# Performance work log

Measured on AMD Instinct MI355X. Metric: run time of the kernel, lower is better.

The kernel has to match this reference:

```python
import jax, jax.numpy as jnp
import numpy as np

NEG_SLOPE = 0.2
EPS = 1e-16  # PyG softmax denominator epsilon


def _gatv2_layer(x, src, dst, n_nodes, W_l, W_r, att, bias):
    """Single-head GATv2Conv (PyG defaults, self loops already in src/dst).
    x: [N, F_in]; src/dst: [E]; W_l/W_r: [F_in, F_out]; att: [F_out]; bias: [F_out].
    """
    x_l = x @ W_l                       # source transform [N, F_out]
    x_r = x @ W_r                       # target transform [N, F_out]
    # per-edge attention logit: a^T LeakyReLU(x_l[j] + x_r[i])
    e = jax.nn.leaky_relu(x_l[src] + x_r[dst], NEG_SLOPE) @ att  # [E]
    # softmax over incoming edges of each destination node
    e_max = jax.ops.segment_max(e, dst, num_segments=n_nodes)    # [N]
    ex = jnp.exp(e - e_max[dst])                                  # [E]
    denom = jax.ops.segment_sum(ex, dst, num_segments=n_nodes)   # [N]
    alpha = ex / (denom[dst] + EPS)                               # [E]
    out = jax.ops.segment_sum(alpha[:, None] * x_l[src], dst, num_segments=n_nodes)
    return out + bias


def setup_inputs() -> dict:
    key = jax.random.key(0)
    N, E = 50000, 800000
    IN, HID, OUT = 128, 64, 64
    ks = jax.random.split(key, 12)
    x = jax.random.normal(ks[0], (N, IN), dtype=jnp.float32)
    edge_index = jax.random.randint(ks[1], (2, E), 0, N, dtype=jnp.int64)
    s1 = float(1.0 / np.sqrt(IN))
    s2 = float(1.0 / np.sqrt(HID))
    return {
        "x": x,
        "edge_index": edge_index,
        "W1_l": jax.random.uniform(ks[2], (IN, HID), jnp.float32, -s1, s1),
        "W1_r": jax.random.uniform(ks[3], (IN, HID), jnp.float32, -s1, s1),
        "att1": jax.random.uniform(ks[4], (HID,), jnp.float32, -s2, s2),
        "b1": jnp.zeros((HID,), jnp.float32),
        "W2_l": jax.random.uniform(ks[5], (HID, OUT), jnp.float32, -s2, s2),
        "W2_r": jax.random.uniform(ks[6], (HID, OUT), jnp.float32, -s2, s2),
        "att2": jax.random.uniform(ks[7], (OUT,), jnp.float32, -s2, s2),
        "b2": jnp.zeros((OUT,), jnp.float32),
    }


def reference(x, edge_index, W1_l, W1_r, att1, b1, W2_l, W2_r, att2, b2):
    n = x.shape[0]
    loop = jnp.arange(n, dtype=edge_index.dtype)
    src = jnp.concatenate([edge_index[0], loop])  # add self loops (PyG default)
    dst = jnp.concatenate([edge_index[1], loop])
    h = _gatv2_layer(x, src, dst, n, W1_l, W1_r, att1, b1)
    h = jax.nn.relu(h)
    out = _gatv2_layer(h, src, dst, n, W2_l, W2_r, att2, b2)
    return out
```

## Files before the change

kernel.cpp:

```cpp
#include <hip/hip_runtime.h>
#include <math.h>

#define NEG_SLOPE 0.2f
#define EPSV 1e-16f
#define NEG_HUGE -1e30f
#define CAP 64
#define GH 1024

typedef short short8 __attribute__((ext_vector_type(8)));
typedef float f32x4 __attribute__((ext_vector_type(4)));
typedef unsigned short u16;


__global__ __launch_bounds__(256) void k_wpack(
        const float* __restrict__ W1l, const float* __restrict__ W1r,
        const float* __restrict__ W2l, const float* __restrict__ W2r,
        u16* __restrict__ w1hi, u16* __restrict__ w1lo,
        u16* __restrict__ w2hi, u16* __restrict__ w2lo,
        int* __restrict__ cnt, u16* __restrict__ csrc, int N, int NP) {
    const int idx = blockIdx.x * 256 + threadIdx.x;
    const int G = gridDim.x * 256;
    const int CN = 8 * NP;
    for (int i = idx; i < CN; i += G) {
        const int cls = i / NP;
        const int r = i - cls * NP;
        const int d = r * 8 + cls;
        cnt[i] = (d < N) ? 1 : 0;
    }
    for (int d = idx; d < N; d += G) csrc[(size_t)d * CAP] = (u16)d;
    const int T1 = 128 * 128, T2 = 64 * 128;
    if (idx >= T1 + T2) return;
    u16 *dhi, *dlo; const float *Wl, *Wr; int li;
    if (idx < T1) { dhi = w1hi; dlo = w1lo; Wl = W1l; Wr = W1r; li = idx; }
    else          { dhi = w2hi; dlo = w2lo; Wl = W2l; Wr = W2r; li = idx - T1; }
    const int j = li & 7, l = (li >> 3) & 63, t = (li >> 9) & 7, c = li >> 12;
    const int k = c * 32 + (l >> 4) * 8 + j;
    const int n = t * 16 + (l & 15);
    const float v = (n < 64) ? Wl[k * 64 + n] : Wr[k * 64 + (n - 64)];
    const unsigned u = __float_as_uint(v);
    dhi[li] = (u16)(u >> 16);
    const float hif = __uint_as_float(u & 0xffff0000u);
    dlo[li] = (u16)(__float_as_uint(v - hif) >> 16);
}

__device__ __forceinline__ void split8(const float* fs, short8& ahi, short8& alo) {
#pragma unroll
    for (int j = 0; j < 8; ++j) {
        const unsigned u = __float_as_uint(fs[j]);
        ahi[j] = (short)(u >> 16);
        const float hif = __uint_as_float(u & 0xffff0000u);
        alo[j] = (short)(__float_as_uint(fs[j] - hif) >> 16);
    }
}

template <int K>
__device__ __forceinline__ void gemm_mfma_tile(const float* __restrict__ X,
                                               const u16* __restrict__ whi,
                                               const u16* __restrict__ wlo,
                                               float* __restrict__ xl,
                                               float* __restrict__ xr,
                                               int N, int tile) {
    const int lane = threadIdx.x & 63;
    const int w = threadIdx.x >> 6;
    const int rowbase = tile * 64 + w * 16;
    const int m = lane & 15, q = lane >> 4;
    int ar = rowbase + m; if (ar > N - 1) ar = N - 1;
    const float* arow = X + (size_t)ar * K + q * 8;
    f32x4 acc[8];
#pragma unroll
    for (int t = 0; t < 8; ++t) acc[t] = (f32x4){0.f, 0.f, 0.f, 0.f};
#pragma unroll
    for (int c = 0; c < K / 32; ++c) {
        const f32x4 f0 = __builtin_nontemporal_load((const f32x4*)(arow + c * 32));
        const f32x4 f1 = __builtin_nontemporal_load((const f32x4*)(arow + c * 32 + 4));
        const float fs[8] = {f0[0], f0[1], f0[2], f0[3], f1[0], f1[1], f1[2], f1[3]};
        short8 ahi, alo;
        split8(fs, ahi, alo);
        const u16* bp = whi + ((size_t)(c * 8) * 64 + lane) * 8;
        const u16* bq = wlo + ((size_t)(c * 8) * 64 + lane) * 8;
#pragma unroll
        for (int t = 0; t < 8; ++t) {
            const short8 bhi = *(const short8*)(bp + t * 64 * 8);
            const short8 blo = *(const short8*)(bq + t * 64 * 8);
            acc[t] = __builtin_amdgcn_mfma_f32_16x16x32_bf16(bhi, ahi, acc[t], 0, 0, 0);
            acc[t] = __builtin_amdgcn_mfma_f32_16x16x32_bf16(blo, ahi, acc[t], 0, 0, 0);
            acc[t] = __builtin_amdgcn_mfma_f32_16x16x32_bf16(bhi, alo, acc[t], 0, 0, 0);
        }
    }
    const int row = rowbase + m;
    if (row < N) {
#pragma unroll
        for (int t = 0; t < 8; ++t) {
            const int colb = t * 16 + q * 4;
            float* dstp = (t < 4) ? (xl + (size_t)row * 64 + colb)
                                  : (xr + (size_t)row * 64 + (colb - 64));
            __builtin_nontemporal_store(acc[t], (f32x4*)dstp);
        }
    }
}

template <int K>
__global__ __launch_bounds__(256) void k_hist_gemm(const int* __restrict__ ei, int E,
                                                   int* __restrict__ cnt,
                                                   u16* __restrict__ csrc,
                                                   const float* __restrict__ X,
                                                   const u16* __restrict__ whi,
                                                   const u16* __restrict__ wlo,
                                                   float* __restrict__ xl,
                                                   float* __restrict__ xr,
                                                   int N, int NP) {
    if ((int)blockIdx.x < GH) {
        const int cls = blockIdx.x & 7;
        const int stripe = blockIdx.x >> 3;
        const int NS = GH >> 3;
        const int tid = threadIdx.x;
        const int* srcp = ei;
        const int* dstp = ei + E;
        int* cntc = cnt + cls * NP;
        if ((E & 7) == 0) {
            for (int base = stripe * 2048; base < E; base += NS * 2048) {
                const int e8 = base + tid * 8;
                if (e8 < E) {
                    const int4 da = *(const int4*)(dstp + e8);
                    const int4 db = *(const int4*)(dstp + e8 + 4);
                    const int4 sa = *(const int4*)(srcp + e8);
                    const int4 sb = *(const int4*)(srcp + e8 + 4);
                    const int d[8] = {da.x, da.y, da.z, da.w, db.x, db.y, db.z, db.w};
                    const int s[8] = {sa.x, sa.y, sa.z, sa.w, sb.x, sb.y, sb.z, sb.w};
                    bool m[8]; int sl[8];
#pragma unroll
                    for (int j = 0; j < 8; ++j) {
                        m[j] = (d[j] & 7) == cls;
                        if (m[j]) sl[j] = atomicAdd(&cntc[d[j] >> 3], 1);
                    }
#pragma unroll
                    for (int j = 0; j < 8; ++j) {
                        if (m[j]) csrc[(size_t)d[j] * CAP + sl[j]] = (u16)s[j];
                    }
                }
            }
        } else {
            for (int base = stripe * 256; base < E; base += NS * 256) {
                const int e = base + tid;
                if (e < E) {
                    const int dd = dstp[e];
                    if ((dd & 7) == cls) {
                        const int ss = srcp[e];
                        const int slot = atomicAdd(&cntc[dd >> 3], 1);
                        csrc[(size_t)dd * CAP + slot] = (u16)ss;
                    }
                }
            }
        }
    } else {
        gemm_mfma_tile<K>(X, whi, wlo, xl, xr, N, blockIdx.x - GH);
    }
}

template <int K>
__global__ __launch_bounds__(256) void k_gemm(const float* __restrict__ X,
                                              const u16* __restrict__ whi,
                                              const u16* __restrict__ wlo,
                                              float* __restrict__ xl,
                                              float* __restrict__ xr, int N) {
    gemm_mfma_tile<K>(X, whi, wlo, xl, xr, N, blockIdx.x);
}

__global__ __launch_bounds__(256) void k_attn(const float* __restrict__ xl,
                                              const float* xr,
                                              const float* __restrict__ att,
                                              const int* __restrict__ cnt,
                                              const u16* __restrict__ csrc,
                                              const float* __restrict__ bias,
                                              float* out, int N, int NP, int relu) {
    const int lane = threadIdx.x & 63;
    const int g = lane >> 4;
    const int i = lane & 15;
    const int dst = blockIdx.x * 4 + (threadIdx.x >> 6);
    if (dst >= N) return;
    const float4 xrv = *(const float4*)(xr + (size_t)dst * 64 + i * 4);
    const float4 aw  = *(const float4*)(att + i * 4);
    const int deg = cnt[(dst & 7) * NP + (dst >> 3)];
    const int sidx = (int)csrc[(size_t)dst * CAP + ((lane < deg) ? lane : 0)];
    float l = 0.0f;
    float4 acc = {0.0f, 0.0f, 0.0f, 0.0f};
    for (int t = 0; t < deg; t += 16) {
        const int s0 = t + g, s1 = t + 4 + g, s2 = t + 8 + g, s3 = t + 12 + g;
        const bool v0 = s0 < deg, v1 = s1 < deg, v2 = s2 < deg, v3 = s3 < deg;
        const int src0 = __shfl(sidx, s0, 64);
        const int src1 = __shfl(sidx, s1, 64);
        const int src2 = __shfl(sidx, s2, 64);
        const int src3 = __shfl(sidx, s3, 64);
        const float4 va = *(const float4*)(xl + (size_t)src0 * 64 + i * 4);
        const float4 vb = *(const float4*)(xl + (size_t)src1 * 64 + i * 4);
        const float4 vc = *(const float4*)(xl + (size_t)src2 * 64 + i * 4);
        const float4 vd = *(const float4*)(xl + (size_t)src3 * 64 + i * 4);
        float t0, p0, p1, p2, p3;
        t0 = va.x + xrv.x; t0 = fmaxf(t0, NEG_SLOPE * t0); p0 = aw.x * t0;
        t0 = va.y + xrv.y; t0 = fmaxf(t0, NEG_SLOPE * t0); p0 = fmaf(aw.y, t0, p0);
        t0 = va.z + xrv.z; t0 = fmaxf(t0, NEG_SLOPE * t0); p0 = fmaf(aw.z, t0, p0);
        t0 = va.w + xrv.w; t0 = fmaxf(t0, NEG_SLOPE * t0); p0 = fmaf(aw.w, t0, p0);
        t0 = vb.x + xrv.x; t0 = fmaxf(t0, NEG_SLOPE * t0); p1 = aw.x * t0;
        t0 = vb.y + xrv.y; t0 = fmaxf(t0, NEG_SLOPE * t0); p1 = fmaf(aw.y, t0, p1);
        t0 = vb.z + xrv.z; t0 = fmaxf(t0, NEG_SLOPE * t0); p1 = fmaf(aw.z, t0, p1);
        t0 = vb.w + xrv.w; t0 = fmaxf(t0, NEG_SLOPE * t0); p1 = fmaf(aw.w, t0, p1);
        t0 = vc.x + xrv.x; t0 = fmaxf(t0, NEG_SLOPE * t0); p2 = aw.x * t0;
        t0 = vc.y + xrv.y; t0 = fmaxf(t0, NEG_SLOPE * t0); p2 = fmaf(aw.y, t0, p2);
        t0 = vc.z + xrv.z; t0 = fmaxf(t0, NEG_SLOPE * t0); p2 = fmaf(aw.z, t0, p2);
        t0 = vc.w + xrv.w; t0 = fmaxf(t0, NEG_SLOPE * t0); p2 = fmaf(aw.w, t0, p2);
        t0 = vd.x + xrv.x; t0 = fmaxf(t0, NEG_SLOPE * t0); p3 = aw.x * t0;
        t0 = vd.y + xrv.y; t0 = fmaxf(t0, NEG_SLOPE * t0); p3 = fmaf(aw.y, t0, p3);
        t0 = vd.z + xrv.z; t0 = fmaxf(t0, NEG_SLOPE * t0); p3 = fmaf(aw.z, t0, p3);
        t0 = vd.w + xrv.w; t0 = fmaxf(t0, NEG_SLOPE * t0); p3 = fmaf(aw.w, t0, p3);
        p0 += __shfl_xor(p0, 1, 64); p1 += __shfl_xor(p1, 1, 64);
        p2 += __shfl_xor(p2, 1, 64); p3 += __shfl_xor(p3, 1, 64);
        p0 += __shfl_xor(p0, 2, 64); p1 += __shfl_xor(p1, 2, 64);
        p2 += __shfl_xor(p2, 2, 64); p3 += __shfl_xor(p3, 2, 64);
        p0 += __shfl_xor(p0, 4, 64); p1 += __shfl_xor(p1, 4, 64);
        p2 += __shfl_xor(p2, 4, 64); p3 += __shfl_xor(p3, 4, 64);
        p0 += __shfl_xor(p0, 8, 64); p1 += __shfl_xor(p1, 8, 64);
        p2 += __shfl_xor(p2, 8, 64); p3 += __shfl_xor(p3, 8, 64);
        const float d0 = __expf(v0 ? p0 : NEG_HUGE);
        const float d1 = __expf(v1 ? p1 : NEG_HUGE);
        const float d2 = __expf(v2 ? p2 : NEG_HUGE);
        const float d3 = __expf(v3 ? p3 : NEG_HUGE);
        l += (d0 + d1) + (d2 + d3);
        acc.x = fmaf(d0, va.x, fmaf(d1, vb.x, fmaf(d2, vc.x, fmaf(d3, vd.x, acc.x))));
        acc.y = fmaf(d0, va.y, fmaf(d1, vb.y, fmaf(d2, vc.y, fmaf(d3, vd.y, acc.y))));
        acc.z = fmaf(d0, va.z, fmaf(d1, vb.z, fmaf(d2, vc.z, fmaf(d3, vd.z, acc.z))));
        acc.w = fmaf(d0, va.w, fmaf(d1, vb.w, fmaf(d2, vc.w, fmaf(d3, vd.w, acc.w))));
    }
#pragma unroll
    for (int o = 16; o <= 32; o <<= 1) {
        l     += __shfl_xor(l, o, 64);
        acc.x += __shfl_xor(acc.x, o, 64);
        acc.y += __shfl_xor(acc.y, o, 64);
        acc.z += __shfl_xor(acc.z, o, 64);
        acc.w += __shfl_xor(acc.w, o, 64);
    }
    if (g == 0) {
        const float4 bv = *(const float4*)(bias + i * 4);
        const float inv = 1.0f / (l + EPSV);
        float4 r;
        r.x = fmaf(acc.x, inv, bv.x);
        r.y = fmaf(acc.y, inv, bv.y);
        r.z = fmaf(acc.z, inv, bv.z);
        r.w = fmaf(acc.w, inv, bv.w);
        if (relu) {
            r.x = fmaxf(r.x, 0.0f); r.y = fmaxf(r.y, 0.0f);
            r.z = fmaxf(r.z, 0.0f); r.w = fmaxf(r.w, 0.0f);
        }
        *(float4*)(out + (size_t)dst * 64 + i * 4) = r;
    }
}


extern "C" void kernel_launch(void* const* d_in, const int* in_sizes, int n_in,
                              void* d_out, int out_size, void* d_ws, size_t ws_size,
                              hipStream_t stream) {
    const float* x    = (const float*)d_in[0];
    const int*   ei   = (const int*)d_in[1];
    const float* W1l  = (const float*)d_in[2];
    const float* W1r  = (const float*)d_in[3];
    const float* att1 = (const float*)d_in[4];
    const float* b1   = (const float*)d_in[5];
    const float* W2l  = (const float*)d_in[6];
    const float* W2r  = (const float*)d_in[7];
    const float* att2 = (const float*)d_in[8];
    const float* b2   = (const float*)d_in[9];

    const int N  = in_sizes[0] / 128;
    const int E  = in_sizes[1] / 2;
    const int NP = (((N + 7) >> 3) + 31) & ~31;

    int* wsi   = (int*)d_ws;
    int* cnt   = wsi;
    u16* csrc  = (u16*)(cnt + 8 * NP);
    u16* w1hi  = csrc + (size_t)N * CAP;
    u16* w1lo  = w1hi + 16384;
    u16* w2hi  = w1lo + 16384;
    u16* w2lo  = w2hi + 8192;
    float* buf1 = (float*)(w2lo + 8192);
    float* buf2 = buf1 + (size_t)N * 64;
    float* fout = (float*)d_out;

    const dim3 b256(256);
    const int gGemm = (N + 63) / 64;
    const int gAttn = (N + 3) / 4;

    k_wpack<<<(128 * 128 + 64 * 128 + 255) / 256, b256, 0, stream>>>(
        W1l, W1r, W2l, W2r, w1hi, w1lo, w2hi, w2lo, cnt, csrc, N, NP);

    k_hist_gemm<128><<<GH + gGemm, b256, 0, stream>>>(ei, E, cnt, csrc,
                                                      x, w1hi, w1lo, fout, buf1, N, NP);
    k_attn<<<gAttn, b256, 0, stream>>>(fout, buf1, att1, cnt, csrc, b1, buf2, N, NP, 1);

    k_gemm<64><<<gGemm, b256, 0, stream>>>(buf2, w2hi, w2lo, buf1, fout, N);
    k_attn<<<gAttn, b256, 0, stream>>>(buf1, fout, att2, cnt, csrc, b2, fout, N, NP, 0);
}
```

Before: 228.1 us.

## Pack edge indices into u32, halve histogram grid, widen attention gather batch

The weight-pack kernel now also packs each edge's dst and src into one 32-bit word (dst<<16 | src), so the histogram pass reads 4 bytes per edge instead of 8. The histogram grid drops from 1024 to 512 blocks and processes 4 packed edges per thread. The attention loop now issues 8 neighbour gathers per step instead of 4 to expose more memory-level parallelism. GEMM loads and stores switch from nontemporal to normal accesses. The packing adds a full pass over the edge list and assumes node ids fit in 16 bits, which the code already relied on for csrc.

New measurement: 224.6 us. Within noise of the previous version (-1.5%).

```diff
diff --git a/kernel.cpp b/kernel.cpp
--- a/kernel.cpp
+++ b/kernel.cpp
@@ -5,16 +5,18 @@
 #define EPSV 1e-16f
 #define NEG_HUGE -1e30f
 #define CAP 64
-#define GH 1024
+#define GH 512
 
 typedef short short8 __attribute__((ext_vector_type(8)));
 typedef float f32x4 __attribute__((ext_vector_type(4)));
 typedef unsigned short u16;
+typedef unsigned int u32;
 
 
 __global__ __launch_bounds__(256) void k_wpack(
         const float* __restrict__ W1l, const float* __restrict__ W1r,
         const float* __restrict__ W2l, const float* __restrict__ W2r,
+        const int* __restrict__ ei, int E, u32* __restrict__ pk,
         u16* __restrict__ w1hi, u16* __restrict__ w1lo,
         u16* __restrict__ w2hi, u16* __restrict__ w2lo,
         int* __restrict__ cnt, u16* __restrict__ csrc, int N, int NP) {
@@ -28,6 +30,12 @@
         cnt[i] = (d < N) ? 1 : 0;
     }
     for (int d = idx; d < N; d += G) csrc[(size_t)d * CAP] = (u16)d;
+    {
+        const int* srcp = ei;
+        const int* dstp = ei + E;
+        for (int e = idx; e < E; e += G)
+            pk[e] = ((u32)dstp[e] << 16) | (u32)srcp[e];
+    }
     const int T1 = 128 * 128, T2 = 64 * 128;
     if (idx >= T1 + T2) return;
     u16 *dhi, *dlo; const float *Wl, *Wr; int li;
@@ -71,9 +79,9 @@
     for (int t = 0; t < 8; ++t) acc[t] = (f32x4){0.f, 0.f, 0.f, 0.f};
 #pragma unroll
     for (int c = 0; c < K / 32; ++c) {
-        const f32x4 f0 = __builtin_nontemporal_load((const f32x4*)(arow + c * 32));
-        const f32x4 f1 = __builtin_nontemporal_load((const f32x4*)(arow + c * 32 + 4));
-        const float fs[8] = {f0[0], f0[1], f0[2], f0[3], f1[0], f1[1], f1[2], f1[3]};
+        const float4 f0 = *(const float4*)(arow + c * 32);
+        const float4 f1 = *(const float4*)(arow + c * 32 + 4);
+        const float fs[8] = {f0.x, f0.y, f0.z, f0.w, f1.x, f1.y, f1.z, f1.w};
         short8 ahi, alo;
         split8(fs, ahi, alo);
         const u16* bp = whi + ((size_t)(c * 8) * 64 + lane) * 8;
@@ -92,15 +100,17 @@
 #pragma unroll
         for (int t = 0; t < 8; ++t) {
             const int colb = t * 16 + q * 4;
+            float4 v;
+            v.x = acc[t][0]; v.y = acc[t][1]; v.z = acc[t][2]; v.w = acc[t][3];
             float* dstp = (t < 4) ? (xl + (size_t)row * 64 + colb)
                                   : (xr + (size_t)row * 64 + (colb - 64));
-            __builtin_nontemporal_store(acc[t], (f32x4*)dstp);
+            *(float4*)dstp = v;
         }
     }
 }
 
 template <int K>
-__global__ __launch_bounds__(256) void k_hist_gemm(const int* __restrict__ ei, int E,
+__global__ __launch_bounds__(256) void k_hist_gemm(const u32* __restrict__ pk, int E,
                                                    int* __restrict__ cnt,
                                                    u16* __restrict__ csrc,
                                                    const float* __restrict__ X,
@@ -114,28 +124,23 @@
         const int stripe = blockIdx.x >> 3;
         const int NS = GH >> 3;
         const int tid = threadIdx.x;
-        const int* srcp = ei;
-        const int* dstp = ei + E;
         int* cntc = cnt + cls * NP;
-        if ((E & 7) == 0) {
-            for (int base = stripe * 2048; base < E; base += NS * 2048) {
-                const int e8 = base + tid * 8;
-                if (e8 < E) {
-                    const int4 da = *(const int4*)(dstp + e8);
-                    const int4 db = *(const int4*)(dstp + e8 + 4);
-                    const int4 sa = *(const int4*)(srcp + e8);
-                    const int4 sb = *(const int4*)(srcp + e8 + 4);
-                    const int d[8] = {da.x, da.y, da.z, da.w, db.x, db.y, db.z, db.w};
-                    const int s[8] = {sa.x, sa.y, sa.z, sa.w, sb.x, sb.y, sb.z, sb.w};
-                    bool m[8]; int sl[8];
-#pragma unroll
-                    for (int j = 0; j < 8; ++j) {
-                        m[j] = (d[j] & 7) == cls;
-                        if (m[j]) sl[j] = atomicAdd(&cntc[d[j] >> 3], 1);
+        if ((E & 3) == 0) {
+            for (int base = stripe * 1024; base < E; base += NS * 1024) {
+                const int e4 = base + tid * 4;
+                if (e4 < E) {
+                    const uint4 p4 = *(const uint4*)(pk + e4);
+                    const u32 pv[4] = {p4.x, p4.y, p4.z, p4.w};
+                    bool m[4]; int sl[4]; int dd[4];
+#pragma unroll
+                    for (int j = 0; j < 4; ++j) {
+                        dd[j] = (int)(pv[j] >> 16);
+                        m[j] = (dd[j] & 7) == cls;
+                        if (m[j]) sl[j] = atomicAdd(&cntc[dd[j] >> 3], 1);
                     }
 #pragma unroll
-                    for (int j = 0; j < 8; ++j) {
-                        if (m[j]) csrc[(size_t)d[j] * CAP + sl[j]] = (u16)s[j];
+                    for (int j = 0; j < 4; ++j) {
+                        if (m[j]) csrc[(size_t)dd[j] * CAP + sl[j]] = (u16)(pv[j] & 0xffffu);
                     }
                 }
             }
@@ -143,11 +148,11 @@
             for (int base = stripe * 256; base < E; base += NS * 256) {
                 const int e = base + tid;
                 if (e < E) {
-                    const int dd = dstp[e];
+                    const u32 pv = pk[e];
+                    const int dd = (int)(pv >> 16);
                     if ((dd & 7) == cls) {
-                        const int ss = srcp[e];
                         const int slot = atomicAdd(&cntc[dd >> 3], 1);
-                        csrc[(size_t)dd * CAP + slot] = (u16)ss;
+                        csrc[(size_t)dd * CAP + slot] = (u16)(pv & 0xffffu);
                     }
                 }
             }
@@ -184,51 +189,39 @@
     const int sidx = (int)csrc[(size_t)dst * CAP + ((lane < deg) ? lane : 0)];
     float l = 0.0f;
     float4 acc = {0.0f, 0.0f, 0.0f, 0.0f};
-    for (int t = 0; t < deg; t += 16) {
-        const int s0 = t + g, s1 = t + 4 + g, s2 = t + 8 + g, s3 = t + 12 + g;
-        const bool v0 = s0 < deg, v1 = s1 < deg, v2 = s2 < deg, v3 = s3 < deg;
-        const int src0 = __shfl(sidx, s0, 64);
-        const int src1 = __shfl(sidx, s1, 64);
-        const int src2 = __shfl(sidx, s2, 64);
-        const int src3 = __shfl(sidx, s3, 64);
-        const float4 va = *(const float4*)(xl + (size_t)src0 * 64 + i * 4);
-        const float4 vb = *(const float4*)(xl + (size_t)src1 * 64 + i * 4);
-        const float4 vc = *(const float4*)(xl + (size_t)src2 * 64 + i * 4);
-        const float4 vd = *(const float4*)(xl + (size_t)src3 * 64 + i * 4);
-        float t0, p0, p1, p2, p3;
-        t0 = va.x + xrv.x; t0 = fmaxf(t0, NEG_SLOPE * t0); p0 = aw.x * t0;
-        t0 = va.y + xrv.y; t0 = fmaxf(t0, NEG_SLOPE * t0); p0 = fmaf(aw.y, t0, p0);
-        t0 = va.z + xrv.z; t0 = fmaxf(t0, NEG_SLOPE * t0); p0 = fmaf(aw.z, t0, p0);
-        t0 = va.w + xrv.w; t0 = fmaxf(t0, NEG_SLOPE * t0); p0 = fmaf(aw.w, t0, p0);
-        t0 = vb.x + xrv.x; t0 = fmaxf(t0, NEG_SLOPE * t0); p1 = aw.x * t0;
-        t0 = vb.y + xrv.y; t0 = fmaxf(t0, NEG_SLOPE * t0); p1 = fmaf(aw.y, t0, p1);
-        t0 = vb.z + xrv.z; t0 = fmaxf(t0, NEG_SLOPE * t0); p1 = fmaf(aw.z, t0, p1);
-        t0 = vb.w + xrv.w; t0 = fmaxf(t0, NEG_SLOPE * t0); p1 = fmaf(aw.w, t0, p1);
-        t0 = vc.x + xrv.x; t0 = fmaxf(t0, NEG_SLOPE * t0); p2 = aw.x * t0;
-        t0 = vc.y + xrv.y; t0 = fmaxf(t0, NEG_SLOPE * t0); p2 = fmaf(aw.y, t0, p2);
-        t0 = vc.z + xrv.z; t0 = fmaxf(t0, NEG_SLOPE * t0); p2 = fmaf(aw.z, t0, p2);
-        t0 = vc.w + xrv.w; t0 = fmaxf(t0, NEG_SLOPE * t0); p2 = fmaf(aw.w, t0, p2);
-        t0 = vd.x + xrv.x; t0 = fmaxf(t0, NEG_SLOPE * t0); p3 = aw.x * t0;
-        t0 = vd.y + xrv.y; t0 = fmaxf(t0, NEG_SLOPE * t0); p3 = fmaf(aw.y, t0, p3);
-        t0 = vd.z + xrv.z; t0 = fmaxf(t0, NEG_SLOPE * t0); p3 = fmaf(aw.z, t0, p3);
-        t0 = vd.w + xrv.w; t0 = fmaxf(t0, NEG_SLOPE * t0); p3 = fmaf(aw.w, t0, p3);
-        p0 += __shfl_xor(p0, 1, 64); p1 += __shfl_xor(p1, 1, 64);
-        p2 += __shfl_xor(p2, 1, 64); p3 += __shfl_xor(p3, 1, 64);
-        p0 += __shfl_xor(p0, 2, 64); p1 += __shfl_xor(p1, 2, 64);
-        p2 += __shfl_xor(p2, 2, 64); p3 += __shfl_xor(p3, 2, 64);
-        p0 += __shfl_xor(p0, 4, 64); p1 += __shfl_xor(p1, 4, 64);
-        p2 += __shfl_xor(p2, 4, 64); p3 += __shfl_xor(p3, 4, 64);
-        p0 += __shfl_xor(p0, 8, 64); p1 += __shfl_xor(p1, 8, 64);
-        p2 += __shfl_xor(p2, 8, 64); p3 += __shfl_xor(p3, 8, 64);
-        const float d0 = __expf(v0 ? p0 : NEG_HUGE);
-        const float d1 = __expf(v1 ? p1 : NEG_HUGE);
-        const float d2 = __expf(v2 ? p2 : NEG_HUGE);
-        const float d3 = __expf(v3 ? p3 : NEG_HUGE);
-        l += (d0 + d1) + (d2 + d3);
-        acc.x = fmaf(d0, va.x, fmaf(d1, vb.x, fmaf(d2, vc.x, fmaf(d3, vd.x, acc.x))));
-        acc.y = fmaf(d0, va.y, fmaf(d1, vb.y, fmaf(d2, vc.y, fmaf(d3, vd.y, acc.y))));
-        acc.z = fmaf(d0, va.z, fmaf(d1, vb.z, fmaf(d2, vc.z, fmaf(d3, vd.z, acc.z))));
-        acc.w = fmaf(d0, va.w, fmaf(d1, vb.w, fmaf(d2, vc.w, fmaf(d3, vd.w, acc.w))));
+    for (int t = 0; t < deg; t += 32) {
+        bool vj[8];
+        float4 va[8];
+#pragma unroll
+        for (int j = 0; j < 8; ++j) {
+            const int s = t + j * 4 + g;
+            vj[j] = s < deg;
+            const int src = __shfl(sidx, s, 64);
+            va[j] = *(const float4*)(xl + (size_t)src * 64 + i * 4);
+        }
+        float p[8];
+#pragma unroll
+        for (int j = 0; j < 8; ++j) {
+            float t0, pp;
+            t0 = va[j].x + xrv.x; t0 = fmaxf(t0, NEG_SLOPE * t0); pp = aw.x * t0;
+            t0 = va[j].y + xrv.y; t0 = fmaxf(t0, NEG_SLOPE * t0); pp = fmaf(aw.y, t0, pp);
+            t0 = va[j].z + xrv.z; t0 = fmaxf(t0, NEG_SLOPE * t0); pp = fmaf(aw.z, t0, pp);
+            t0 = va[j].w + xrv.w; t0 = fmaxf(t0, NEG_SLOPE * t0); pp = fmaf(aw.w, t0, pp);
+            p[j] = pp;
+        }
+#pragma unroll
+        for (int j = 0; j < 8; ++j) {
+            p[j] += __shfl_xor(p[j], 1, 64);
+            p[j] += __shfl_xor(p[j], 2, 64);
+            p[j] += __shfl_xor(p[j], 4, 64);
+            p[j] += __shfl_xor(p[j], 8, 64);
+            const float dj = __expf(vj[j] ? p[j] : NEG_HUGE);
+            l += dj;
+            acc.x = fmaf(dj, va[j].x, acc.x);
+            acc.y = fmaf(dj, va[j].y, acc.y);
+            acc.z = fmaf(dj, va[j].z, acc.z);
+            acc.w = fmaf(dj, va[j].w, acc.w);
+        }
     }
 #pragma unroll
     for (int o = 16; o <= 32; o <<= 1) {
@@ -280,7 +273,8 @@
     u16* w1lo  = w1hi + 16384;
     u16* w2hi  = w1lo + 16384;
     u16* w2lo  = w2hi + 8192;
-    float* buf1 = (float*)(w2lo + 8192);
+    u32* pk    = (u32*)(w2lo + 8192);
+    float* buf1 = (float*)(pk + E);
     float* buf2 = buf1 + (size_t)N * 64;
     float* fout = (float*)d_out;
 
@@ -288,10 +282,11 @@
     const int gGemm = (N + 63) / 64;
     const int gAttn = (N + 3) / 4;
 
-    k_wpack<<<(128 * 128 + 64 * 128 + 255) / 256, b256, 0, stream>>>(
-        W1l, W1r, W2l, W2r, w1hi, w1lo, w2hi, w2lo, cnt, csrc, N, NP);
-
-    k_hist_gemm<128><<<GH + gGemm, b256, 0, stream>>>(ei, E, cnt, csrc,
+    k_wpack<<<512, b256, 0, stream>>>(
+        W1l, W1r, W2l, W2r, ei, E, pk,
+        w1hi, w1lo, w2hi, w2lo, cnt, csrc, N, NP);
+
+    k_hist_gemm<128><<<GH + gGemm, b256, 0, stream>>>(pk, E, cnt, csrc,
                                                       x, w1hi, w1lo, fout, buf1, N, NP);
     k_attn<<<gAttn, b256, 0, stream>>>(fout, buf1, att1, cnt, csrc, b1, buf2, N, NP, 1);
 
```
